# Optimization experiments

Measured on AMD Instinct MI355X. Metric: run time of the kernel, lower is better.

Reference implementation:

```python
import jax, jax.numpy as jnp
import numpy as np

T, B, V = 50, 128, 8000          # seq_len, batch, inputDimSize
A = 728                          # numAncestors
NEMB = V + A                     # rows of W_emb
E, H, ATT, C, L = 128, 128, 100, 283, 5


def setup_inputs() -> dict:
    key = jax.random.key(0)
    ks = jax.random.split(key, 12)
    x = jax.random.normal(ks[0], (T, B, V), jnp.float32)
    mask = jnp.ones((T, B), jnp.float32)
    leaves = jax.random.randint(ks[1], (V, L), 0, NEMB)
    ancestors = jax.random.randint(ks[2], (V, L), 0, NEMB)
    W_emb = jax.random.uniform(ks[3], (NEMB, E), jnp.float32)
    W_attention = jax.random.uniform(ks[4], (2 * E, ATT), jnp.float32)
    b_attention = jnp.zeros((ATT,), jnp.float32)
    v_attention = jax.random.uniform(ks[5], (ATT,), jnp.float32)
    gru_w_ih = jax.random.normal(ks[6], (3 * H, E), jnp.float32) * 0.1
    gru_w_hh = jax.random.normal(ks[7], (3 * H, H), jnp.float32) * 0.1
    gru_b_ih = jnp.zeros((3 * H,), jnp.float32)
    gru_b_hh = jnp.zeros((3 * H,), jnp.float32)
    W_output = jax.random.uniform(ks[8], (H, C), jnp.float32) * 0.1
    b_output = jnp.zeros((C,), jnp.float32)
    return {"x": x, "mask": mask, "W_emb": W_emb,
            "W_attention": W_attention, "b_attention": b_attention,
            "v_attention": v_attention, "gru_w_ih": gru_w_ih,
            "gru_w_hh": gru_w_hh, "gru_b_ih": gru_b_ih,
            "gru_b_hh": gru_b_hh, "W_output": W_output,
            "b_output": b_output, "leaves": leaves, "ancestors": ancestors}


def reference(x, mask, W_emb, W_attention, b_attention, v_attention,
              gru_w_ih, gru_w_hh, gru_b_ih, gru_b_hh,
              W_output, b_output, leaves, ancestors):
    # --- Attention over ontology ancestors (gather + MLP + softmax + reduce) ---
    le = W_emb[leaves]       # [V, L, E]
    an = W_emb[ancestors]    # [V, L, E]
    att_in = jnp.concatenate([le, an], axis=-1)              # [V, L, 2E]
    mlp = jnp.tanh(att_in @ W_attention + b_attention)       # [V, L, ATT]
    pre = mlp @ v_attention                                  # [V, L]
    att = jax.nn.softmax(pre, axis=1)                        # softmax over ancestors
    emb = jnp.einsum('vle,vl->ve', an, att)                  # [V, E]

    # --- project multi-hot visits into embedding space ---
    x_emb = jnp.tanh(jnp.einsum('tbv,ve->tbe', x, emb))      # [T, B, E]

    # --- torch-style single-layer GRU via scan (time-major) ---
    def cell(h, xt):
        gx = xt @ gru_w_ih.T + gru_b_ih                      # [B, 3H]
        gh = h @ gru_w_hh.T + gru_b_hh
        xr, xz, xn = jnp.split(gx, 3, axis=-1)
        hr, hz, hn = jnp.split(gh, 3, axis=-1)
        r = jax.nn.sigmoid(xr + hr)
        z = jax.nn.sigmoid(xz + hz)
        n = jnp.tanh(xn + r * hn)
        h_new = (1.0 - z) * n + z * h
        return h_new, h_new

    h0 = jnp.zeros((B, H), x_emb.dtype)
    _, hidden = jax.lax.scan(cell, h0, x_emb)                # [T, B, H]

    # dropout_rate = 0 -> identity
    # exp / sum == softmax over the class dim
    out = jax.nn.softmax(hidden @ W_output + b_output, axis=2)  # [T, B, C]
    return out * mask[:, :, None]
```

## Files before the change

### kernel.cpp

```cpp
#include <hip/hip_runtime.h>


typedef unsigned short u16;
typedef unsigned int   u32;
typedef short bf16x8 __attribute__((ext_vector_type(8)));
typedef float f32x4  __attribute__((ext_vector_type(4)));

typedef __attribute__((address_space(1))) u32 gas_u32;
typedef __attribute__((address_space(3))) u32 las_u32;

union U4 { u32 u[4]; bf16x8 v; uint4 q; };

__device__ __forceinline__ float uaf(u32 u){ union{u32 u; float f;} c; c.u=u; return c.f; }
__device__ __forceinline__ u32 fau(float f){ union{u32 u; float f;} c; c.f=f; return c.u; }
__device__ __forceinline__ u16 f2bf(float f){ u32 u=fau(f); return (u16)((u + 0x7fffu + ((u>>16)&1u))>>16); }
__device__ __forceinline__ float sigm(float x){ return 1.f/(1.f+__expf(-x)); }

__device__ __forceinline__ void gll16(const void* g, void* l){
    __builtin_amdgcn_global_load_lds((const gas_u32*)g, (las_u32*)l, 16, 0, 0);
}

__device__ __forceinline__ void split8(const float* f, bf16x8* hi, bf16x8* lo){
    U4 H, L;
    #pragma unroll
    for (int j=0;j<4;++j){
        float f0=f[2*j], f1=f[2*j+1];
        u32 u0=fau(f0), u1=fau(f1);
        u32 t0=u0+0x7fffu+((u0>>16)&1u);
        u32 t1=u1+0x7fffu+((u1>>16)&1u);
        u32 h1=t1&0xffff0000u;
        H.u[j]=(t0>>16)|h1;
        float l0=f0-uaf(t0&0xffff0000u);
        float l1=f1-uaf(h1);
        u32 v0=fau(l0), v1=fau(l1);
        u32 s0=v0+0x7fffu+((v0>>16)&1u);
        u32 s1=v1+0x7fffu+((v1>>16)&1u);
        L.u[j]=(s0>>16)|(s1&0xffff0000u);
    }
    *hi=H.v; *lo=L.v;
}

__device__ __forceinline__ void split1(float f, u16& h, u16& l){
    u32 u=fau(f); u32 t=u+0x7fffu+((u>>16)&1u); h=(u16)(t>>16);
    float lf=f-uaf(t&0xffff0000u); l=f2bf(lf);
}

#define MFMA(a,b,c) __builtin_amdgcn_mfma_f32_16x16x32_bf16(a,b,c,0,0,0)

__global__ __launch_bounds__(256,1) void prep_watt_kernel(
    const float* __restrict__ W_att, u16* __restrict__ WT_h, u16* __restrict__ WT_l)
{
    int n=blockIdx.x, k=threadIdx.x;
    float f = (n<100)? W_att[k*100+n] : 0.f;
    u16 h,l; split1(f,h,l);
    WT_h[n*256+k]=h; WT_l[n*256+k]=l;
}

__global__ __launch_bounds__(256,1) void prep_whh_kernel(
    const float* __restrict__ whh, u32* __restrict__ out)
{
    int i=blockIdx.x*256+threadIdx.x;
    int j=i>>6, p=i&63;
    u32 a=(u32)f2bf(whh[j*128+2*p]);
    u32 b=(u32)f2bf(whh[j*128+2*p+1]);
    out[i]=a|(b<<16);
}

__global__ __launch_bounds__(256,1) void transpose_wih_kernel(
    const float* __restrict__ w_ih, float* __restrict__ w_ihT)
{
    int i=blockIdx.x*256+threadIdx.x;
    int e=i/384, j=i-e*384;
    w_ihT[i]=w_ih[j*128+e];
}

__global__ __launch_bounds__(256,1) void attn_mlp_kernel(
    const float* __restrict__ W_emb, const float* __restrict__ b_att,
    const float* __restrict__ v_att, const int* __restrict__ leaves,
    const int* __restrict__ anc, const u16* __restrict__ WT_h,
    const u16* __restrict__ WT_l, float* __restrict__ emb_f)
{
    __shared__ __align__(16) char smem[61440];
    short* Ah=(short*)smem;
    short* Al=(short*)(smem+16384);
    short* Bh=(short*)(smem+32768);
    short* Bl=(short*)(smem+47104);
    float* mlp_s=(float*)smem;
    __shared__ float s_pre[128];
    __shared__ float s_vatt[112];
    __shared__ float s_attw[128];
    __shared__ int   s_leaf[128], s_anc[128];

    const int tid=threadIdx.x;
    const int wave=tid>>6, lane=tid&63;
    const int vb5=blockIdx.x*125;

    if (tid<125){ s_leaf[tid]=leaves[vb5+tid]; s_anc[tid]=anc[vb5+tid]; }
    else if (tid<128){ s_leaf[tid]=leaves[vb5]; s_anc[tid]=anc[vb5]; }
    if (tid<100) s_vatt[tid]=v_att[tid];

    f32x4 acc[2][7];
    const f32x4 zf={0.f,0.f,0.f,0.f};
    #pragma unroll
    for (int mi=0;mi<2;++mi)
        #pragma unroll
        for (int ni=0;ni<7;++ni) acc[mi][ni]=zf;

    const int fr=lane&15, fq=lane>>4;

    for (int kc=0;kc<4;++kc){
        __syncthreads();
        {
            int r=tid>>1, seg=tid&1;
            int src=(kc<2)? s_leaf[r] : s_anc[r];
            const float* srcp = W_emb + (size_t)src*128 + (kc&1)*64 + seg*32;
            float buf[32];
            #pragma unroll
            for (int i=0;i<8;++i) *(f32x4*)(buf+4*i) = *(const f32x4*)(srcp+4*i);
            #pragma unroll
            for (int j=0;j<4;++j){
                bf16x8 hv, lv; split8(buf+8*j, &hv, &lv);
                U4 H,L; H.v=hv; L.v=lv;
                *(uint4*)&Ah[r*64+seg*32+j*8] = H.q;
                *(uint4*)&Al[r*64+seg*32+j*8] = L.q;
            }
        }
        for (int c=wave;c<14;c+=4){
            size_t go=(size_t)(c*8+(lane>>3))*512 + (size_t)kc*128 + (size_t)(lane&7)*16;
            gll16((const char*)WT_h+go, Bh+c*512);
            gll16((const char*)WT_l+go, Bl+c*512);
        }
        __syncthreads();

        #pragma unroll
        for (int ks=0;ks<2;++ks){
            bf16x8 ah[2],al[2],bh[7],bl[7];
            #pragma unroll
            for (int mi=0;mi<2;++mi){
                int row=wave*32+mi*16+fr;
                ah[mi]=*(const bf16x8*)&Ah[row*64+ks*32+fq*8];
                al[mi]=*(const bf16x8*)&Al[row*64+ks*32+fq*8];
            }
            #pragma unroll
            for (int ni=0;ni<7;++ni){
                int rowb=ni*16+fr;
                bh[ni]=*(const bf16x8*)&Bh[rowb*64+ks*32+fq*8];
                bl[ni]=*(const bf16x8*)&Bl[rowb*64+ks*32+fq*8];
            }
            #pragma unroll
            for (int mi=0;mi<2;++mi)
                #pragma unroll
                for (int ni=0;ni<7;++ni){
                    acc[mi][ni]=MFMA(ah[mi],bh[ni],acc[mi][ni]);
                    acc[mi][ni]=MFMA(ah[mi],bl[ni],acc[mi][ni]);
                    acc[mi][ni]=MFMA(al[mi],bh[ni],acc[mi][ni]);
                }
        }
    }
    __syncthreads();
    #pragma unroll
    for (int ni=0;ni<7;++ni){
        int col=ni*16+fr;
        float bb=(col<100)? b_att[col] : 0.f;
        #pragma unroll
        for (int mi=0;mi<2;++mi){
            int rb=wave*32+mi*16+fq*4;
            #pragma unroll
            for (int r=0;r<4;++r)
                mlp_s[(rb+r)*112+col]=tanhf(acc[mi][ni][r]+bb);
        }
    }
    __syncthreads();
    if (tid<128){
        float s=0.f;
        for (int n=0;n<100;++n) s+=mlp_s[tid*112+n]*s_vatt[n];
        s_pre[tid]=s;
    }
    __syncthreads();
    if (tid<25){
        float p[5], mx=-1e30f;
        #pragma unroll
        for (int l=0;l<5;++l){ p[l]=s_pre[tid*5+l]; mx=fmaxf(mx,p[l]); }
        float s=0.f;
        #pragma unroll
        for (int l=0;l<5;++l){ p[l]=__expf(p[l]-mx); s+=p[l]; }
        float inv=1.f/s;
        #pragma unroll
        for (int l=0;l<5;++l) s_attw[tid*5+l]=p[l]*inv;
    }
    __syncthreads();
    for (int o=tid;o<3200;o+=256){
        int v=o>>7, e=o&127;
        float s=0.f;
        #pragma unroll
        for (int l=0;l<5;++l)
            s += s_attw[v*5+l]*W_emb[(size_t)s_anc[v*5+l]*128+e];
        emb_f[(size_t)(blockIdx.x*25+v)*128+e]=s;
    }
}

__global__ __launch_bounds__(256,1) void emb_split_kernel(
    const float* __restrict__ emb_f, u16* __restrict__ hiT, u16* __restrict__ loT)
{
    __shared__ float tile[64*128];
    const int tid=threadIdx.x;
    const int vb=blockIdx.x*64;
    for (int i=tid;i<2048;i+=256){
        int row=i>>5, q=i&31;
        *(f32x4*)&tile[row*128+q*4] = *(const f32x4*)&emb_f[(size_t)(vb+row)*128+q*4];
    }
    __syncthreads();
    u32* hw=(u32*)hiT; u32* lw=(u32*)loT;
    for (int o=tid;o<4096;o+=256){
        int e=o>>5, p=o&31;
        float f0=tile[(2*p)*128+e], f1=tile[(2*p+1)*128+e];
        u16 h0,l0,h1,l1; split1(f0,h0,l0); split1(f1,h1,l1);
        size_t base=(size_t)e*4000 + (size_t)(vb>>1) + p;
        hw[base]=(u32)h0|((u32)h1<<16);
        lw[base]=(u32)l0|((u32)l1<<16);
    }
}

__global__ __launch_bounds__(256,4) void gemm_xemb_kernel(
    const float* __restrict__ x, const u16* __restrict__ bhT, const u16* __restrict__ blT,
    float* __restrict__ partials)
{
    __shared__ __align__(16) short Ah[32*64];
    __shared__ __align__(16) short Al[32*64];
    __shared__ __align__(16) short Bh[128*64];
    __shared__ __align__(16) short Bl[128*64];

    const int tid=threadIdx.x, wave=tid>>6, lane=tid&63;
    const int mt=blockIdx.x%200, ks=blockIdx.x/200;
    const int mbase=mt*32;
    const int k0=ks*1600;

    f32x4 acc[2][2];
    const f32x4 zf={0.f,0.f,0.f,0.f};
    #pragma unroll
    for (int i=0;i<2;++i)
        #pragma unroll
        for (int j=0;j<2;++j) acc[i][j]=zf;

    const char* bhb=(const char*)bhT;
    const char* blb=(const char*)blT;
    const int fr=lane&15, fq=lane>>4;
    const int nbase=wave*32;

    const int sr=tid>>3, sc=tid&7;
    const float* agp = x + (size_t)(mbase+sr)*8000 + k0 + sc*8;
    bf16x8* awh = (bf16x8*)&Ah[sr*64 + ((sc^(sr&7))<<3)];
    bf16x8* awl = (bf16x8*)&Al[sr*64 + ((sc^(sr&7))<<3)];

    const int br=lane>>3, bc0=lane&7;

    f32x4 pa0 = *(const f32x4*)agp;
    f32x4 pa1 = *(const f32x4*)(agp+4);

    for (int kk=k0; kk<k0+1600; kk+=64){
        __syncthreads();
        {
            float buf[8];
            *(f32x4*)&buf[0]=pa0; *(f32x4*)&buf[4]=pa1;
            bf16x8 hv,lv; split8(buf,&hv,&lv);
            *awh=hv; *awl=lv;
        }
        #pragma unroll
        for (int ii=0;ii<4;++ii){
            int s=wave*4+ii;
            int r=s*8+br;
            int c=bc0^(r&7);
            size_t go=((size_t)r*8000 + kk + c*8)*2;
            gll16(bhb+go, (char*)Bh + (size_t)s*1024);
            gll16(blb+go, (char*)Bl + (size_t)s*1024);
        }
        __syncthreads();

        if (kk+64 < k0+1600){
            const float* ag = agp + (kk + 64 - k0);
            pa0=*(const f32x4*)ag; pa1=*(const f32x4*)(ag+4);
        }

        #pragma unroll
        for (int kh=0;kh<2;++kh){
            bf16x8 ah[2],al[2],bh[2],bl[2];
            #pragma unroll
            for (int mi=0;mi<2;++mi){
                int row=mi*16+fr;
                int ci=(kh*4+fq)^(row&7);
                ah[mi]=*(const bf16x8*)&Ah[row*64+ci*8];
                al[mi]=*(const bf16x8*)&Al[row*64+ci*8];
            }
            #pragma unroll
            for (int ni=0;ni<2;++ni){
                int rowb=nbase+ni*16+fr;
                int ch=rowb*8+((kh*4+fq)^(rowb&7));
                bh[ni]=*(const bf16x8*)&Bh[ch*8];
                bl[ni]=*(const bf16x8*)&Bl[ch*8];
            }
            #pragma unroll
            for (int mi=0;mi<2;++mi)
                #pragma unroll
                for (int ni=0;ni<2;++ni){
                    acc[mi][ni]=MFMA(ah[mi],bh[ni],acc[mi][ni]);
                    acc[mi][ni]=MFMA(ah[mi],bl[ni],acc[mi][ni]);
                    acc[mi][ni]=MFMA(al[mi],bh[ni],acc[mi][ni]);
                }
        }
    }

    float* pout=partials + ((size_t)ks*6400+mbase)*128;
    #pragma unroll
    for (int mi=0;mi<2;++mi)
        #pragma unroll
        for (int ni=0;ni<2;++ni)
            #pragma unroll
            for (int r=0;r<4;++r)
                pout[(size_t)(mi*16+fq*4+r)*128 + nbase+ni*16+fr]=acc[mi][ni][r];
}

__global__ __launch_bounds__(384,2) void sumtanh_gx_kernel(
    const float* __restrict__ partials, const float* __restrict__ w_ihT,
    const float* __restrict__ b_ih, float* __restrict__ GX)
{
    __shared__ float sx[2048];
    const int tid=threadIdx.x;
    const int rb=blockIdx.x*16;
    for (int i=tid;i<2048;i+=384){
        size_t o=(size_t)rb*128+i;
        float s=0.f;
        #pragma unroll
        for (int k=0;k<5;++k) s+=partials[(size_t)k*819200+o];
        sx[i]=tanhf(s);
    }
    __syncthreads();

    float acc[16];
    #pragma unroll
    for (int r=0;r<16;++r) acc[r]=0.f;
    for (int e=0;e<128;++e){
        float w0=w_ihT[e*384+tid];
        #pragma unroll
        for (int r=0;r<16;++r) acc[r]=fmaf(sx[r*128+e],w0,acc[r]);
    }
    float b0=b_ih[tid];
    #pragma unroll
    for (int r=0;r<16;++r)
        GX[(size_t)(rb+r)*384+tid]=acc[r]+b0;
}

__global__ __launch_bounds__(384,1) void gru_scan_kernel(
    const u32* __restrict__ whh_p, const float* __restrict__ b_hh,
    const float* __restrict__ GX, float* __restrict__ hidden)
{
    __shared__ __align__(16) u16 shb[128];
    __shared__ float sgh[384];
    const int tid=threadIdx.x, b=blockIdx.x;

    float wf[128];
    #pragma unroll
    for (int q=0;q<64;++q){
        u32 u=whh_p[tid*64+q];
        wf[2*q]  =uaf(u<<16);
        wf[2*q+1]=uaf(u&0xffff0000u);
    }
    float hreg=0.f;
    if (tid<128) shb[tid]=0;
    const float bb=b_hh[tid];

    float gx0=0.f,gx1=0.f,gx2=0.f;
    if (tid<128){
        const float* gp=GX+(size_t)b*384;
        gx0=gp[tid]; gx1=gp[128+tid]; gx2=gp[256+tid];
    }
    __syncthreads();

    for (int t=0;t<50;++t){
        float nx0=0.f,nx1=0.f,nx2=0.f;
        if (tid<128 && t<49){
            const float* gp=GX+((size_t)(t+1)*128+b)*384;
            nx0=gp[tid]; nx1=gp[128+tid]; nx2=gp[256+tid];
        }
        float acc=0.f;
        #pragma unroll
        for (int p=0;p<16;++p){
            U4 c; c.v=*(const bf16x8*)&shb[p*8];
            #pragma unroll
            for (int j=0;j<4;++j){
                u32 u=c.u[j];
                acc=fmaf(uaf(u<<16),         wf[p*8+2*j],   acc);
                acc=fmaf(uaf(u&0xffff0000u), wf[p*8+2*j+1], acc);
            }
        }
        sgh[tid]=acc+bb;
        __syncthreads();
        if (tid<128){
            float r=sigm(gx0+sgh[tid]);
            float z=sigm(gx1+sgh[128+tid]);
            float n=tanhf(gx2+r*sgh[256+tid]);
            float hn=(1.f-z)*n+z*hreg;
            hreg=hn;
            hidden[((size_t)t*128+b)*128+tid]=hn;
            shb[tid]=f2bf(hn);
        }
        __syncthreads();
        gx0=nx0; gx1=nx1; gx2=nx2;
    }
}

__global__ __launch_bounds__(320,2) void logits_softmax_kernel(
    const float* __restrict__ hidden, const float* __restrict__ W_out,
    const float* __restrict__ b_out, const float* __restrict__ mask,
    float* __restrict__ out)
{
    __shared__ float shd[2048];
    __shared__ float slog[16*288];
    const int tid=threadIdx.x;
    const int rb=blockIdx.x*16;
    for (int i=tid;i<2048;i+=320) shd[i]=hidden[(size_t)rb*128+i];
    __syncthreads();

    const bool act=(tid<283);
    const int cl=act? tid : 282;
    float acc[16];
    #pragma unroll
    for (int r=0;r<16;++r) acc[r]=0.f;
    for (int h=0;h<128;++h){
        float w0=W_out[h*283+cl];
        #pragma unroll
        for (int r=0;r<16;++r) acc[r]=fmaf(shd[r*128+h],w0,acc[r]);
    }
    float b0=b_out[cl];
    if (act){
        #pragma unroll
        for (int r=0;r<16;++r) slog[r*288+tid]=acc[r]+b0;
    }
    __syncthreads();

    const int wv=tid>>6, lane=tid&63;
    if (wv<4){
        #pragma unroll
        for (int rr=0;rr<4;++rr){
            int r=wv*4+rr;
            int m=rb+r;
            float v[5];
            float mx=-1e30f;
            #pragma unroll
            for (int i=0;i<5;++i){
                int c=lane+i*64;
                v[i]=(c<283)? slog[r*288+c] : -1e30f;
                mx=fmaxf(mx,v[i]);
            }
            #pragma unroll
            for (int off=32;off>0;off>>=1) mx=fmaxf(mx,__shfl_xor(mx,off,64));
            float s=0.f;
            #pragma unroll
            for (int i=0;i<5;++i){
                int c=lane+i*64;
                v[i]=(c<283)? __expf(v[i]-mx) : 0.f;
                s+=v[i];
            }
            #pragma unroll
            for (int off=32;off>0;off>>=1) s+=__shfl_xor(s,off,64);
            const float sc=mask[m]/s;
            float* op=out+(size_t)m*283;
            #pragma unroll
            for (int i=0;i<5;++i){
                int c=lane+i*64;
                if (c<283) op[c]=v[i]*sc;
            }
        }
    }
}

extern "C" void kernel_launch(void* const* d_in, const int* in_sizes, int n_in,
                              void* d_out, int out_size, void* d_ws, size_t ws_size,
                              hipStream_t stream) {
    const float* x      = (const float*)d_in[0];
    const float* mask   = (const float*)d_in[1];
    const float* W_emb  = (const float*)d_in[2];
    const float* W_att  = (const float*)d_in[3];
    const float* b_att  = (const float*)d_in[4];
    const float* v_att  = (const float*)d_in[5];
    const float* w_ih   = (const float*)d_in[6];
    const float* w_hh   = (const float*)d_in[7];
    const float* b_ih   = (const float*)d_in[8];
    const float* b_hh   = (const float*)d_in[9];
    const float* W_out  = (const float*)d_in[10];
    const float* b_out  = (const float*)d_in[11];
    const int* leaves   = (const int*)d_in[12];
    const int* anc      = (const int*)d_in[13];
    float* out = (float*)d_out;

    char* w = (char*)d_ws;
    u16*   WT_h    = (u16*)(w + 0);
    u16*   WT_l    = (u16*)(w + 57344);
    u32*   whh_p   = (u32*)(w + 114688);
    float* w_ihT   = (float*)(w + 212992);
    u16*   emb_hiT = (u16*)(w + 409600);
    u16*   emb_loT = (u16*)(w + 2457600);
    float* emb_f   = (float*)(w + 4505600);
    float* partials= (float*)(w + 8601600);
    float* GX      = (float*)(w + 24985600);
    float* hidden  = (float*)(w + 34816000);

    prep_watt_kernel<<<112, 256, 0, stream>>>(W_att, WT_h, WT_l);
    prep_whh_kernel<<<96, 256, 0, stream>>>(w_hh, whh_p);
    transpose_wih_kernel<<<192, 256, 0, stream>>>(w_ih, w_ihT);
    attn_mlp_kernel<<<320, 256, 0, stream>>>(W_emb, b_att, v_att, leaves, anc,
                                             WT_h, WT_l, emb_f);
    emb_split_kernel<<<125, 256, 0, stream>>>(emb_f, emb_hiT, emb_loT);
    gemm_xemb_kernel<<<1000, 256, 0, stream>>>(x, emb_hiT, emb_loT, partials);
    sumtanh_gx_kernel<<<400, 384, 0, stream>>>(partials, w_ihT, b_ih, GX);
    gru_scan_kernel<<<128, 384, 0, stream>>>(whh_p, b_hh, GX, hidden);
    logits_softmax_kernel<<<400, 320, 0, stream>>>(hidden, W_out, b_out, mask, out);
}
```

Measured before the change: 474.2 us.

## Double GEMM M-tile to 64 rows and merge three prep kernels

The x·emb GEMM now processes 64 rows of x per block instead of 32, halving the block count so each loaded emb (B) tile is reused across twice as many rows. This cuts redundant B-tile traffic, at the cost of more registers and LDS per block (launch bounds lowered to 3 blocks per CU) and fewer blocks. The three small weight-preparation kernels are also fused into one launch that dispatches on block index, removing two kernel launches.

```diff
diff --git a/kernel.cpp b/kernel.cpp
--- a/kernel.cpp
+++ b/kernel.cpp
@@ -47,31 +47,28 @@
 
 #define MFMA(a,b,c) __builtin_amdgcn_mfma_f32_16x16x32_bf16(a,b,c,0,0,0)
 
-__global__ __launch_bounds__(256,1) void prep_watt_kernel(
-    const float* __restrict__ W_att, u16* __restrict__ WT_h, u16* __restrict__ WT_l)
-{
-    int n=blockIdx.x, k=threadIdx.x;
-    float f = (n<100)? W_att[k*100+n] : 0.f;
-    u16 h,l; split1(f,h,l);
-    WT_h[n*256+k]=h; WT_l[n*256+k]=l;
-}
-
-__global__ __launch_bounds__(256,1) void prep_whh_kernel(
-    const float* __restrict__ whh, u32* __restrict__ out)
-{
-    int i=blockIdx.x*256+threadIdx.x;
-    int j=i>>6, p=i&63;
-    u32 a=(u32)f2bf(whh[j*128+2*p]);
-    u32 b=(u32)f2bf(whh[j*128+2*p+1]);
-    out[i]=a|(b<<16);
-}
-
-__global__ __launch_bounds__(256,1) void transpose_wih_kernel(
+__global__ __launch_bounds__(256,1) void prep_kernel(
+    const float* __restrict__ W_att, u16* __restrict__ WT_h, u16* __restrict__ WT_l,
+    const float* __restrict__ whh, u32* __restrict__ whh_p,
     const float* __restrict__ w_ih, float* __restrict__ w_ihT)
 {
-    int i=blockIdx.x*256+threadIdx.x;
-    int e=i/384, j=i-e*384;
-    w_ihT[i]=w_ih[j*128+e];
+    const int bid=blockIdx.x, tid=threadIdx.x;
+    if (bid<112){
+        int n=bid, k=tid;
+        float f=(n<100)? W_att[k*100+n] : 0.f;
+        u16 h,l; split1(f,h,l);
+        WT_h[n*256+k]=h; WT_l[n*256+k]=l;
+    } else if (bid<208){
+        int i=(bid-112)*256+tid;
+        int j=i>>6, p=i&63;
+        u32 a=(u32)f2bf(whh[j*128+2*p]);
+        u32 b=(u32)f2bf(whh[j*128+2*p+1]);
+        whh_p[i]=a|(b<<16);
+    } else {
+        int i=(bid-208)*256+tid;
+        int e=i/384, j=i-e*384;
+        w_ihT[i]=w_ih[j*128+e];
+    }
 }
 
 __global__ __launch_bounds__(256,1) void attn_mlp_kernel(
@@ -221,24 +218,24 @@
     }
 }
 
-__global__ __launch_bounds__(256,4) void gemm_xemb_kernel(
+__global__ __launch_bounds__(256,3) void gemm_xemb_kernel(
     const float* __restrict__ x, const u16* __restrict__ bhT, const u16* __restrict__ blT,
     float* __restrict__ partials)
 {
-    __shared__ __align__(16) short Ah[32*64];
-    __shared__ __align__(16) short Al[32*64];
+    __shared__ __align__(16) short Ah[64*64];
+    __shared__ __align__(16) short Al[64*64];
     __shared__ __align__(16) short Bh[128*64];
     __shared__ __align__(16) short Bl[128*64];
 
     const int tid=threadIdx.x, wave=tid>>6, lane=tid&63;
-    const int mt=blockIdx.x%200, ks=blockIdx.x/200;
-    const int mbase=mt*32;
+    const int mt=blockIdx.x%100, ks=blockIdx.x/100;
+    const int mbase=mt*64;
     const int k0=ks*1600;
 
-    f32x4 acc[2][2];
+    f32x4 acc[4][2];
     const f32x4 zf={0.f,0.f,0.f,0.f};
     #pragma unroll
-    for (int i=0;i<2;++i)
+    for (int i=0;i<4;++i)
         #pragma unroll
         for (int j=0;j<2;++j) acc[i][j]=zf;
 
@@ -247,23 +244,27 @@
     const int fr=lane&15, fq=lane>>4;
     const int nbase=wave*32;
 
-    const int sr=tid>>3, sc=tid&7;
+    const int sr=tid>>2, sc=(tid&3)*2;
     const float* agp = x + (size_t)(mbase+sr)*8000 + k0 + sc*8;
-    bf16x8* awh = (bf16x8*)&Ah[sr*64 + ((sc^(sr&7))<<3)];
-    bf16x8* awl = (bf16x8*)&Al[sr*64 + ((sc^(sr&7))<<3)];
+    bf16x8* awh0=(bf16x8*)&Ah[sr*64 + (((sc  )^(sr&7))<<3)];
+    bf16x8* awl0=(bf16x8*)&Al[sr*64 + (((sc  )^(sr&7))<<3)];
+    bf16x8* awh1=(bf16x8*)&Ah[sr*64 + (((sc+1)^(sr&7))<<3)];
+    bf16x8* awl1=(bf16x8*)&Al[sr*64 + (((sc+1)^(sr&7))<<3)];
 
     const int br=lane>>3, bc0=lane&7;
 
-    f32x4 pa0 = *(const f32x4*)agp;
-    f32x4 pa1 = *(const f32x4*)(agp+4);
+    f32x4 pa0=*(const f32x4*)agp,     pa1=*(const f32x4*)(agp+4);
+    f32x4 pa2=*(const f32x4*)(agp+8), pa3=*(const f32x4*)(agp+12);
 
     for (int kk=k0; kk<k0+1600; kk+=64){
         __syncthreads();
         {
             float buf[8];
+            bf16x8 hv,lv;
             *(f32x4*)&buf[0]=pa0; *(f32x4*)&buf[4]=pa1;
-            bf16x8 hv,lv; split8(buf,&hv,&lv);
-            *awh=hv; *awl=lv;
+            split8(buf,&hv,&lv); *awh0=hv; *awl0=lv;
+            *(f32x4*)&buf[0]=pa2; *(f32x4*)&buf[4]=pa3;
+            split8(buf,&hv,&lv); *awh1=hv; *awl1=lv;
         }
         #pragma unroll
         for (int ii=0;ii<4;++ii){
@@ -277,15 +278,16 @@
         __syncthreads();
 
         if (kk+64 < k0+1600){
-            const float* ag = agp + (kk + 64 - k0);
-            pa0=*(const f32x4*)ag; pa1=*(const f32x4*)(ag+4);
+            const float* ag = agp + (kk+64-k0);
+            pa0=*(const f32x4*)ag;     pa1=*(const f32x4*)(ag+4);
+            pa2=*(const f32x4*)(ag+8); pa3=*(const f32x4*)(ag+12);
         }
 
         #pragma unroll
         for (int kh=0;kh<2;++kh){
-            bf16x8 ah[2],al[2],bh[2],bl[2];
-            #pragma unroll
-            for (int mi=0;mi<2;++mi){
+            bf16x8 ah[4],al[4],bh[2],bl[2];
+            #pragma unroll
+            for (int mi=0;mi<4;++mi){
                 int row=mi*16+fr;
                 int ci=(kh*4+fq)^(row&7);
                 ah[mi]=*(const bf16x8*)&Ah[row*64+ci*8];
@@ -299,7 +301,7 @@
                 bl[ni]=*(const bf16x8*)&Bl[ch*8];
             }
             #pragma unroll
-            for (int mi=0;mi<2;++mi)
+            for (int mi=0;mi<4;++mi)
                 #pragma unroll
                 for (int ni=0;ni<2;++ni){
                     acc[mi][ni]=MFMA(ah[mi],bh[ni],acc[mi][ni]);
@@ -311,7 +313,7 @@
 
     float* pout=partials + ((size_t)ks*6400+mbase)*128;
     #pragma unroll
-    for (int mi=0;mi<2;++mi)
+    for (int mi=0;mi<4;++mi)
         #pragma unroll
         for (int ni=0;ni<2;++ni)
             #pragma unroll
@@ -504,13 +506,11 @@
     float* GX      = (float*)(w + 24985600);
     float* hidden  = (float*)(w + 34816000);
 
-    prep_watt_kernel<<<112, 256, 0, stream>>>(W_att, WT_h, WT_l);
-    prep_whh_kernel<<<96, 256, 0, stream>>>(w_hh, whh_p);
-    transpose_wih_kernel<<<192, 256, 0, stream>>>(w_ih, w_ihT);
+    prep_kernel<<<400, 256, 0, stream>>>(W_att, WT_h, WT_l, w_hh, whh_p, w_ih, w_ihT);
     attn_mlp_kernel<<<320, 256, 0, stream>>>(W_emb, b_att, v_att, leaves, anc,
                                              WT_h, WT_l, emb_f);
     emb_split_kernel<<<125, 256, 0, stream>>>(emb_f, emb_hiT, emb_loT);
-    gemm_xemb_kernel<<<1000, 256, 0, stream>>>(x, emb_hiT, emb_loT, partials);
+    gemm_xemb_kernel<<<500, 256, 0, stream>>>(x, emb_hiT, emb_loT, partials);
     sumtanh_gx_kernel<<<400, 384, 0, stream>>>(partials, w_ihT, b_ih, GX);
     gru_scan_kernel<<<128, 384, 0, stream>>>(whh_p, b_hh, GX, hidden);
     logits_softmax_kernel<<<400, 320, 0, stream>>>(hidden, W_out, b_out, mask, out);
```

Measured after the change: 462.4 us. -2.5%, faster.
